# Kernel tuning notes

Measured on AMD Instinct MI355X. Metric: run time of the kernel, lower is better.

## Reference

```python
import math
import jax, jax.numpy as jnp
import numpy as np

B, C, H, W = 4, 256, 64, 64
N_HEAD = 4
GROUPS = 32
EPS = 1e-5


def setup_inputs() -> dict:
    key = jax.random.key(0)
    k1, k2, k3 = jax.random.split(key, 3)
    fan = C  # 1x1 conv fan_in
    bound_qkv = math.sqrt(3.0 * 1.0 / ((fan + 3 * C) / 2))
    x = jax.random.normal(k1, (B, C, H, W), dtype=jnp.float32)
    w_qkv = jax.random.uniform(k2, (3 * C, C), dtype=jnp.float32, minval=-bound_qkv, maxval=bound_qkv)
    # out conv has scale=1e-10 init, but use small random weights for a non-trivial baseline
    w_out = jax.random.normal(k3, (C, C), dtype=jnp.float32) * 0.02
    return {
        "x": x,
        "gn_gamma": jnp.ones((C,), jnp.float32),
        "gn_beta": jnp.zeros((C,), jnp.float32),
        "w_qkv": w_qkv,
        "b_qkv": jnp.zeros((3 * C,), jnp.float32),
        "w_out": w_out,
        "b_out": jnp.zeros((C,), jnp.float32),
    }


def _group_norm(x, gamma, beta):
    b, c, h, w = x.shape
    xr = x.reshape(b, GROUPS, c // GROUPS, h, w)
    mean = xr.mean(axis=(2, 3, 4), keepdims=True)
    var = xr.var(axis=(2, 3, 4), keepdims=True)
    xn = ((xr - mean) * jax.lax.rsqrt(var + EPS)).reshape(b, c, h, w)
    return xn * gamma[None, :, None, None] + beta[None, :, None, None]


def reference(x, gn_gamma, gn_beta, w_qkv, b_qkv, w_out, b_out):
    b, c, h, w = x.shape
    head_dim = c // N_HEAD
    norm = _group_norm(x, gn_gamma, gn_beta)
    # 1x1 conv == channel matmul
    qkv = jnp.einsum('oc,bchw->bohw', w_qkv, norm) + b_qkv[None, :, None, None]
    qkv = qkv.reshape(b, N_HEAD, 3 * head_dim, h, w)
    q, k, v = jnp.split(qkv, 3, axis=2)  # each [b, n, d, h, w]
    # note: original scales by sqrt(channel), NOT sqrt(head_dim)
    attn = jnp.einsum('bnchw,bncyx->bnhwyx', q, k) / math.sqrt(c)
    attn = jax.nn.softmax(attn.reshape(b, N_HEAD, h, w, h * w), axis=-1)
    attn = attn.reshape(b, N_HEAD, h, w, h, w)
    out = jnp.einsum('bnhwyx,bncyx->bnchw', attn, v).reshape(b, c, h, w)
    out = jnp.einsum('oc,bchw->bohw', w_out, out) + b_out[None, :, None, None]
    return (out + x) / np.sqrt(2.0).astype(np.float32)
```

## Files before the change

kernel.cpp:

```cpp
#include <hip/hip_runtime.h>
#include <hip/hip_bf16.h>

#define B_   4
#define C_   256
#define HW_  4096
#define GR_  32
#define CPG_ 8
#define EPS_ 1e-5f
#define QSCALE_ 0.09016844005555897f
#define RSQRT2_ 0.70710678118654752f

typedef short bf16x8 __attribute__((ext_vector_type(8)));
typedef short bf16x4 __attribute__((ext_vector_type(4)));
typedef float f32x4  __attribute__((ext_vector_type(4)));
typedef unsigned short u16x4 __attribute__((ext_vector_type(4)));
typedef unsigned int u32x4 __attribute__((ext_vector_type(4)));

__device__ __forceinline__ unsigned short f2bf(float f) {
  unsigned int x; __builtin_memcpy(&x, &f, 4);
  x = x + 0x7FFFu + ((x >> 16) & 1u);
  return (unsigned short)(x >> 16);
}
__device__ __forceinline__ unsigned int cvtpk(float lo, float hi) {
  unsigned int r;
  asm("v_cvt_pk_bf16_f32 %0, %1, %2" : "=v"(r) : "v"(lo), "v"(hi));
  return r;
}
__device__ __forceinline__ float exp2v(float x) {
  float r;
  asm("v_exp_f32 %0, %1" : "=v"(r) : "v"(x));
  return r;
}

#define GP(p) ((const __attribute__((address_space(1))) void*)(p))
#define LP(p) ((__attribute__((address_space(3))) void*)(p))

__global__ __launch_bounds__(256) void wcvt(const float* __restrict__ wqkv,
                                            const float* __restrict__ bqkv,
                                            const float* __restrict__ wout,
                                            unsigned short* __restrict__ wbf,
                                            float* __restrict__ bias_s) {
  int i = blockIdx.x * 256 + threadIdx.x;
  const int NQ = 768 * 256, NO = 256 * 256;
  if (i < NQ) {
    int o = i >> 8;
    float s = ((o % 192) < 64) ? QSCALE_ : 1.0f;
    wbf[i] = f2bf(wqkv[i] * s);
  } else if (i < NQ + NO) {
    wbf[i] = f2bf(wout[i - NQ]);
  } else if (i < NQ + NO + 768) {
    int o = i - NQ - NO;
    float s = ((o % 192) < 64) ? QSCALE_ : 1.0f;
    bias_s[o] = bqkv[o] * s;
  }
}

__global__ __launch_bounds__(256) void gn_stats(const float* __restrict__ x,
                                                float* __restrict__ stats) {
  int bg = blockIdx.x;
  const float4* p = (const float4*)(x + (size_t)bg * (CPG_ * HW_));
  float s = 0.f, ss = 0.f;
  for (int i = threadIdx.x; i < (CPG_ * HW_ / 4); i += 256) {
    float4 v = p[i];
    s  += v.x + v.y + v.z + v.w;
    ss += v.x * v.x + v.y * v.y + v.z * v.z + v.w * v.w;
  }
  #pragma unroll
  for (int off = 32; off > 0; off >>= 1) {
    s  += __shfl_down(s, off, 64);
    ss += __shfl_down(ss, off, 64);
  }
  __shared__ float rs[4], rss[4];
  int wv = threadIdx.x >> 6;
  if ((threadIdx.x & 63) == 0) { rs[wv] = s; rss[wv] = ss; }
  __syncthreads();
  if (threadIdx.x == 0) {
    float S = rs[0] + rs[1] + rs[2] + rs[3];
    float SS = rss[0] + rss[1] + rss[2] + rss[3];
    float mean = S * (1.f / (CPG_ * HW_));
    float var = SS * (1.f / (CPG_ * HW_)) - mean * mean;
    stats[bg * 2 + 0] = mean;
    stats[bg * 2 + 1] = rsqrtf(var + EPS_);
  }
}

__global__ __launch_bounds__(256) void gn_apply_t(const float* __restrict__ x,
                                                  const float* __restrict__ stats,
                                                  const float* __restrict__ gamma,
                                                  const float* __restrict__ beta,
                                                  unsigned short* __restrict__ xnt) {
  int p0 = blockIdx.x * 64;
  int c0 = blockIdx.y * 64;
  int b  = blockIdx.z;
  int t = threadIdx.x;
  int cl16 = t & 15;
  int row16 = t >> 4;
  __shared__ unsigned short tile[64][66];
  #pragma unroll
  for (int i = 0; i < 4; ++i) {
    int c = c0 + i * 16 + row16;
    int bg = b * GR_ + (c >> 3);
    float mean = stats[bg * 2], rstd = stats[bg * 2 + 1];
    float a = rstd * gamma[c];
    float bb = beta[c] - mean * a;
    float4 v = *(const float4*)&x[((size_t)(b * C_ + c)) * HW_ + p0 + cl16 * 4];
    u16x4 o;
    o[0] = f2bf(v.x * a + bb); o[1] = f2bf(v.y * a + bb);
    o[2] = f2bf(v.z * a + bb); o[3] = f2bf(v.w * a + bb);
    *(u16x4*)&tile[i * 16 + row16][cl16 * 4] = o;
  }
  __syncthreads();
  #pragma unroll
  for (int i = 0; i < 4; ++i) {
    int pp = i * 16 + row16;
    u16x4 o;
    #pragma unroll
    for (int k = 0; k < 4; ++k) o[k] = tile[cl16 * 4 + k][pp];
    *(u16x4*)&xnt[((size_t)b * HW_ + p0 + pp) * C_ + c0 + cl16 * 4] = o;
  }
}

__global__ __launch_bounds__(512) void gemm_qkv(const unsigned short* __restrict__ wbf,
                                                const float* __restrict__ bias_s,
                                                const unsigned short* __restrict__ xnt,
                                                unsigned short* __restrict__ qt,
                                                unsigned short* __restrict__ ktb,
                                                unsigned short* __restrict__ vb) {
  int p0 = blockIdx.x * 64;
  int b  = blockIdx.y;
  int lane = threadIdx.x & 63, wv = threadIdx.x >> 6;
  int cl = lane & 15, g = lane >> 4;

  __shared__ unsigned short bt[64 * 256];

  {
    const unsigned short* xb = xnt + ((size_t)b * HW_ + p0) * C_;
    int rowl = lane >> 5;
    int grl  = lane & 31;
    #pragma unroll
    for (int i = 0; i < 4; ++i) {
      int row = wv * 8 + i * 2 + rowl;
      int sgr = grl ^ (row & 7);
      __builtin_amdgcn_global_load_lds(GP(xb + (size_t)row * C_ + sgr * 8),
                                       LP(bt + (wv * 8 + i * 2) * C_), 16, 0, 0);
    }
  }
  __syncthreads();

  f32x4 z = {0.f, 0.f, 0.f, 0.f};
  f32x4 acc[6][4];
  #pragma unroll
  for (int j = 0; j < 6; ++j)
    #pragma unroll
    for (int nt = 0; nt < 4; ++nt) acc[j][nt] = z;

  const char* btc = (const char*)bt;
  for (int kc = 0; kc < C_; kc += 32) {
    bf16x8 bfr[4];
    #pragma unroll
    for (int nt = 0; nt < 4; ++nt) {
      int row = nt * 16 + cl;
      bfr[nt] = *(const bf16x8*)(btc + row * 512 + ((((kc >> 3) + g) ^ (cl & 7)) << 4));
    }
    #pragma unroll
    for (int j = 0; j < 6; ++j) {
      int rt = wv * 6 + j;
      bf16x8 af = *(const bf16x8*)&wbf[(size_t)(rt * 16 + cl) * C_ + kc + g * 8];
      #pragma unroll
      for (int nt = 0; nt < 4; ++nt)
        acc[j][nt] = __builtin_amdgcn_mfma_f32_16x16x32_bf16(af, bfr[nt], acc[j][nt], 0, 0, 0);
    }
  }

  #pragma unroll
  for (int j = 0; j < 6; ++j) {
    int rt = wv * 6 + j;
    int y = rt >> 2;
    int h = y / 3, type = y - h * 3;
    int bh = b * 4 + h;
    int olocal = (rt & 3) * 16 + g * 4;
    int obase = rt * 16 + g * 4;
    if (type == 2) {
      unsigned short* dst = vb + (size_t)bh * 64 * HW_;
      #pragma unroll
      for (int r = 0; r < 4; ++r) {
        float bv = bias_s[obase + r];
        #pragma unroll
        for (int nt = 0; nt < 4; ++nt)
          dst[(size_t)(olocal + r) * HW_ + p0 + nt * 16 + cl] = f2bf(acc[j][nt][r] + bv);
      }
    } else {
      unsigned short* dst = (type == 0 ? qt : ktb) + (size_t)bh * HW_ * 64;
      #pragma unroll
      for (int nt = 0; nt < 4; ++nt) {
        int p = p0 + nt * 16 + cl;
        u16x4 o4;
        #pragma unroll
        for (int r = 0; r < 4; ++r) o4[r] = f2bf(acc[j][nt][r] + bias_s[obase + r]);
        *(u16x4*)&dst[(size_t)p * 64 + olocal] = o4;
      }
    }
  }
}

__global__ __launch_bounds__(512) void flash_attn(const unsigned short* __restrict__ qt,
                                                  const unsigned short* __restrict__ ktb,
                                                  const unsigned short* __restrict__ vb,
                                                  unsigned short* __restrict__ attnt) {
  int qtile = blockIdx.x;
  int bh = blockIdx.y;
  int lane = threadIdx.x & 63, wv = threadIdx.x >> 6;
  int cl = lane & 15, g = lane >> 4;
  int r8 = lane >> 3;
  int gi = (lane & 7) ^ r8;

  const unsigned short* qtb = qt  + (size_t)bh * HW_ * 64;
  const unsigned short* ktp = ktb + (size_t)bh * HW_ * 64;
  const unsigned short* vbp = vb  + (size_t)bh * 64 * HW_;

  __shared__ unsigned short smem[2][8192];

  int qpix0 = qtile * 256 + wv * 32 + cl;
  bf16x8 qf0[2], qf1[2];
  qf0[0] = *(const bf16x8*)&qtb[(size_t)qpix0 * 64 + g * 8];
  qf0[1] = *(const bf16x8*)&qtb[(size_t)qpix0 * 64 + 32 + g * 8];
  qf1[0] = *(const bf16x8*)&qtb[(size_t)(qpix0 + 16) * 64 + g * 8];
  qf1[1] = *(const bf16x8*)&qtb[(size_t)(qpix0 + 16) * 64 + 32 + g * 8];

  f32x4 z = {0.f, 0.f, 0.f, 0.f};
  f32x4 oacc0[4] = {z, z, z, z};
  f32x4 oacc1[4] = {z, z, z, z};
  f32x4 lfrag0 = z, lfrag1 = z;
  const bf16x4 ones = {(short)0x3F80, (short)0x3F80, (short)0x3F80, (short)0x3F80};

  int rdo = cl * 128 + ((g * 16) ^ ((cl & 7) << 4));
  int vbase = cl * 128 + (g & 1) * 8;
  int vxor  = (cl & 7) << 4;
  int ghalf = g >> 1;

  const unsigned short* kp = ktp + (size_t)(wv * 8 + r8) * 64 + gi * 8;
  const unsigned short* vp = vbp + (size_t)(wv * 8 + r8) * HW_ + gi * 8;

#define STAGE(bi) do {                                                              \
    unsigned short* sb = &smem[bi][0];                                              \
    __builtin_amdgcn_global_load_lds(GP(kp), LP(sb + wv * 512),        16, 0, 0);   \
    __builtin_amdgcn_global_load_lds(GP(vp), LP(sb + 4096 + wv * 512), 16, 0, 0);   \
    kp += 64 * 64;                                                                  \
    vp += 64;                                                                       \
  } while (0)

  STAGE(0);
  __syncthreads();

  int cur = 0;
  for (int t = 0; t < 64; ++t) {
    if (t < 63) STAGE(cur ^ 1);

    const char* kb  = (const char*)&smem[cur][0];
    const char* vbx = (const char*)&smem[cur][4096];

    f32x4 sacc0[4] = {z, z, z, z};
    f32x4 sacc1[4] = {z, z, z, z};
    __builtin_amdgcn_s_setprio(1);
    #pragma unroll
    for (int nt = 0; nt < 4; ++nt) {
      #pragma unroll
      for (int ks = 0; ks < 2; ++ks) {
        bf16x8 kf = *(const bf16x8*)(kb + rdo + nt * 2048 + ks * 64);
        sacc0[nt] = __builtin_amdgcn_mfma_f32_16x16x32_bf16(kf, qf0[ks], sacc0[nt], 0, 0, 0);
        sacc1[nt] = __builtin_amdgcn_mfma_f32_16x16x32_bf16(kf, qf1[ks], sacc1[nt], 0, 0, 0);
      }
    }
    __builtin_amdgcn_s_setprio(0);

    unsigned int pk01a[4], pk23a[4], pk01b[4], pk23b[4];
    #pragma unroll
    for (int nt = 0; nt < 4; ++nt) {
      pk01a[nt] = cvtpk(exp2v(sacc0[nt][0]), exp2v(sacc0[nt][1]));
      pk23a[nt] = cvtpk(exp2v(sacc0[nt][2]), exp2v(sacc0[nt][3]));
      pk01b[nt] = cvtpk(exp2v(sacc1[nt][0]), exp2v(sacc1[nt][1]));
      pk23b[nt] = cvtpk(exp2v(sacc1[nt][2]), exp2v(sacc1[nt][3]));
    }

    __builtin_amdgcn_s_setprio(1);
    #pragma unroll
    for (int nt = 0; nt < 4; ++nt) {
      union { unsigned int u[2]; bf16x4 v; } pb0, pb1;
      pb0.u[0] = pk01a[nt]; pb0.u[1] = pk23a[nt];
      pb1.u[0] = pk01b[nt]; pb1.u[1] = pk23b[nt];
      lfrag0 = __builtin_amdgcn_mfma_f32_16x16x16bf16_1k(ones, pb0.v, lfrag0, 0, 0, 0);
      lfrag1 = __builtin_amdgcn_mfma_f32_16x16x16bf16_1k(ones, pb1.v, lfrag1, 0, 0, 0);
      int gsw = ((nt * 2 + ghalf) << 4) ^ vxor;
      #pragma unroll
      for (int dt = 0; dt < 4; ++dt) {
        bf16x4 vf = *(const bf16x4*)(vbx + dt * 2048 + vbase + gsw);
        oacc0[dt] = __builtin_amdgcn_mfma_f32_16x16x16bf16_1k(vf, pb0.v, oacc0[dt], 0, 0, 0);
        oacc1[dt] = __builtin_amdgcn_mfma_f32_16x16x16bf16_1k(vf, pb1.v, oacc1[dt], 0, 0, 0);
      }
    }
    __builtin_amdgcn_s_setprio(0);
    __syncthreads();
    cur ^= 1;
  }
#undef STAGE

  int b = bh >> 2, h = bh & 3;
  float rl0 = 1.f / lfrag0[0];
  float rl1 = 1.f / lfrag1[0];
  unsigned short* at0 = attnt + ((size_t)b * HW_ + qpix0) * C_ + h * 64;
  unsigned short* at1 = attnt + ((size_t)b * HW_ + qpix0 + 16) * C_ + h * 64;
  #pragma unroll
  for (int dt = 0; dt < 4; ++dt) {
    u16x4 o4a, o4b;
    #pragma unroll
    for (int r = 0; r < 4; ++r) {
      o4a[r] = f2bf(oacc0[dt][r] * rl0);
      o4b[r] = f2bf(oacc1[dt][r] * rl1);
    }
    *(u16x4*)&at0[dt * 16 + g * 4] = o4a;
    *(u16x4*)&at1[dt * 16 + g * 4] = o4b;
  }
}

__global__ __launch_bounds__(512) void gemm_out(const unsigned short* __restrict__ wbf_out,
                                                const float* __restrict__ bias,
                                                const unsigned short* __restrict__ attnt,
                                                const float* __restrict__ x,
                                                float* __restrict__ out) {
  int p0 = blockIdx.x * 64;
  int b  = blockIdx.y;
  int lane = threadIdx.x & 63, wv = threadIdx.x >> 6;
  int cl = lane & 15, g = lane >> 4;

  __shared__ unsigned short bt[64 * 256];

  {
    const unsigned short* ab = attnt + ((size_t)b * HW_ + p0) * C_;
    int rowl = lane >> 5;
    int grl  = lane & 31;
    #pragma unroll
    for (int i = 0; i < 4; ++i) {
      int row = wv * 8 + i * 2 + rowl;
      int sgr = grl ^ (row & 7);
      __builtin_amdgcn_global_load_lds(GP(ab + (size_t)row * C_ + sgr * 8),
                                       LP(bt + (wv * 8 + i * 2) * C_), 16, 0, 0);
    }
  }
  __syncthreads();

  f32x4 z = {0.f, 0.f, 0.f, 0.f};
  f32x4 acc[2][4];
  #pragma unroll
  for (int j = 0; j < 2; ++j)
    #pragma unroll
    for (int nt = 0; nt < 4; ++nt) acc[j][nt] = z;

  const char* btc = (const char*)bt;
  for (int kc = 0; kc < C_; kc += 32) {
    bf16x8 bfr[4];
    #pragma unroll
    for (int nt = 0; nt < 4; ++nt) {
      int row = nt * 16 + cl;
      bfr[nt] = *(const bf16x8*)(btc + row * 512 + ((((kc >> 3) + g) ^ (cl & 7)) << 4));
    }
    #pragma unroll
    for (int j = 0; j < 2; ++j) {
      int rt = wv * 2 + j;
      bf16x8 af = *(const bf16x8*)&wbf_out[(size_t)(rt * 16 + cl) * C_ + kc + g * 8];
      #pragma unroll
      for (int nt = 0; nt < 4; ++nt)
        acc[j][nt] = __builtin_amdgcn_mfma_f32_16x16x32_bf16(af, bfr[nt], acc[j][nt], 0, 0, 0);
    }
  }

  const float* xb = x + (size_t)b * C_ * HW_;
  float* ob = out + (size_t)b * C_ * HW_;
  #pragma unroll
  for (int j = 0; j < 2; ++j) {
    int rt = wv * 2 + j;
    #pragma unroll
    for (int r = 0; r < 4; ++r) {
      int o = rt * 16 + g * 4 + r;
      float bv = bias[o];
      #pragma unroll
      for (int nt = 0; nt < 4; ++nt) {
        int p = p0 + nt * 16 + cl;
        size_t idx = (size_t)o * HW_ + p;
        ob[idx] = (acc[j][nt][r] + bv + xb[idx]) * RSQRT2_;
      }
    }
  }
}

extern "C" void kernel_launch(void* const* d_in, const int* in_sizes, int n_in,
                              void* d_out, int out_size, void* d_ws, size_t ws_size,
                              hipStream_t stream) {
  const float* x     = (const float*)d_in[0];
  const float* gamma = (const float*)d_in[1];
  const float* beta  = (const float*)d_in[2];
  const float* w_qkv = (const float*)d_in[3];
  const float* b_qkv = (const float*)d_in[4];
  const float* w_out = (const float*)d_in[5];
  const float* b_out = (const float*)d_in[6];
  float* out = (float*)d_out;

  char* ws = (char*)d_ws;
  float* stats           = (float*)ws;
  float* bias_s          = (float*)(ws + 1024);
  unsigned short* wbf    = (unsigned short*)(ws + 4096);
  unsigned short* xnt    = (unsigned short*)(ws + 528384);
  unsigned short* qt     = (unsigned short*)(ws + 8916992);
  unsigned short* ktb    = (unsigned short*)(ws + 17305600);
  unsigned short* vb     = (unsigned short*)(ws + 25694208);
  unsigned short* attnt  = xnt;

  wcvt<<<dim3(1028), dim3(256), 0, stream>>>(w_qkv, b_qkv, w_out, wbf, bias_s);
  gn_stats<<<dim3(128), dim3(256), 0, stream>>>(x, stats);
  gn_apply_t<<<dim3(64, 4, 4), dim3(256), 0, stream>>>(x, stats, gamma, beta, xnt);
  gemm_qkv<<<dim3(64, 4), dim3(512), 0, stream>>>(wbf, bias_s, xnt, qt, ktb, vb);
  flash_attn<<<dim3(16, 16), dim3(512), 0, stream>>>(qt, ktb, vb, attnt);
  gemm_out<<<dim3(64, 4), dim3(512), 0, stream>>>(wbf + 768 * 256, b_out, attnt, x, out);
}
```

Measured before the change: 146.6 us.

## Fuse GroupNorm apply into QKV GEMM and compute softmax denominator with VALU adds

```diff
diff --git a/kernel.cpp b/kernel.cpp
--- a/kernel.cpp
+++ b/kernel.cpp
@@ -84,45 +84,12 @@
   }
 }
 
-__global__ __launch_bounds__(256) void gn_apply_t(const float* __restrict__ x,
-                                                  const float* __restrict__ stats,
-                                                  const float* __restrict__ gamma,
-                                                  const float* __restrict__ beta,
-                                                  unsigned short* __restrict__ xnt) {
-  int p0 = blockIdx.x * 64;
-  int c0 = blockIdx.y * 64;
-  int b  = blockIdx.z;
-  int t = threadIdx.x;
-  int cl16 = t & 15;
-  int row16 = t >> 4;
-  __shared__ unsigned short tile[64][66];
-  #pragma unroll
-  for (int i = 0; i < 4; ++i) {
-    int c = c0 + i * 16 + row16;
-    int bg = b * GR_ + (c >> 3);
-    float mean = stats[bg * 2], rstd = stats[bg * 2 + 1];
-    float a = rstd * gamma[c];
-    float bb = beta[c] - mean * a;
-    float4 v = *(const float4*)&x[((size_t)(b * C_ + c)) * HW_ + p0 + cl16 * 4];
-    u16x4 o;
-    o[0] = f2bf(v.x * a + bb); o[1] = f2bf(v.y * a + bb);
-    o[2] = f2bf(v.z * a + bb); o[3] = f2bf(v.w * a + bb);
-    *(u16x4*)&tile[i * 16 + row16][cl16 * 4] = o;
-  }
-  __syncthreads();
-  #pragma unroll
-  for (int i = 0; i < 4; ++i) {
-    int pp = i * 16 + row16;
-    u16x4 o;
-    #pragma unroll
-    for (int k = 0; k < 4; ++k) o[k] = tile[cl16 * 4 + k][pp];
-    *(u16x4*)&xnt[((size_t)b * HW_ + p0 + pp) * C_ + c0 + cl16 * 4] = o;
-  }
-}
-
 __global__ __launch_bounds__(512) void gemm_qkv(const unsigned short* __restrict__ wbf,
                                                 const float* __restrict__ bias_s,
-                                                const unsigned short* __restrict__ xnt,
+                                                const float* __restrict__ x,
+                                                const float* __restrict__ stats,
+                                                const float* __restrict__ gamma,
+                                                const float* __restrict__ beta,
                                                 unsigned short* __restrict__ qt,
                                                 unsigned short* __restrict__ ktb,
                                                 unsigned short* __restrict__ vb) {
@@ -132,20 +99,44 @@
   int cl = lane & 15, g = lane >> 4;
 
   __shared__ unsigned short bt[64 * 256];
+  __shared__ unsigned short scratch[64][68];
 
   {
-    const unsigned short* xb = xnt + ((size_t)b * HW_ + p0) * C_;
-    int rowl = lane >> 5;
-    int grl  = lane & 31;
-    #pragma unroll
-    for (int i = 0; i < 4; ++i) {
-      int row = wv * 8 + i * 2 + rowl;
-      int sgr = grl ^ (row & 7);
-      __builtin_amdgcn_global_load_lds(GP(xb + (size_t)row * C_ + sgr * 8),
-                                       LP(bt + (wv * 8 + i * 2) * C_), 16, 0, 0);
-    }
-  }
-  __syncthreads();
+    int t = threadIdx.x;
+    int cl16 = t & 15;
+    int row32 = t >> 4;
+    const float* xb = x + (size_t)b * C_ * HW_;
+    #pragma unroll
+    for (int cc = 0; cc < 4; ++cc) {
+      int c0 = cc * 64;
+      #pragma unroll
+      for (int i = 0; i < 2; ++i) {
+        int cloc = i * 32 + row32;
+        int c = c0 + cloc;
+        int bg = b * GR_ + (c >> 3);
+        float mean = stats[bg * 2], rstd = stats[bg * 2 + 1];
+        float a = rstd * gamma[c];
+        float bb = beta[c] - mean * a;
+        float4 v = *(const float4*)&xb[(size_t)c * HW_ + p0 + cl16 * 4];
+        u16x4 o;
+        o[0] = f2bf(v.x * a + bb); o[1] = f2bf(v.y * a + bb);
+        o[2] = f2bf(v.z * a + bb); o[3] = f2bf(v.w * a + bb);
+        *(u16x4*)&scratch[cloc][cl16 * 4] = o;
+      }
+      __syncthreads();
+      #pragma unroll
+      for (int i = 0; i < 2; ++i) {
+        int pp = i * 32 + row32;
+        u16x4 o;
+        #pragma unroll
+        for (int k = 0; k < 4; ++k) o[k] = scratch[cl16 * 4 + k][pp];
+        int cbyte = (c0 + cl16 * 4) * 2;
+        int sw = (((cbyte >> 4) ^ (pp & 7)) << 4) | (cbyte & 15);
+        *(u16x4*)((char*)bt + pp * 512 + sw) = o;
+      }
+      __syncthreads();
+    }
+  }
 
   f32x4 z = {0.f, 0.f, 0.f, 0.f};
   f32x4 acc[6][4];
@@ -230,8 +221,7 @@
   f32x4 z = {0.f, 0.f, 0.f, 0.f};
   f32x4 oacc0[4] = {z, z, z, z};
   f32x4 oacc1[4] = {z, z, z, z};
-  f32x4 lfrag0 = z, lfrag1 = z;
-  const bf16x4 ones = {(short)0x3F80, (short)0x3F80, (short)0x3F80, (short)0x3F80};
+  f32x4 lacc0 = z, lacc1 = z;
 
   int rdo = cl * 128 + ((g * 16) ^ ((cl & 7) << 4));
   int vbase = cl * 128 + (g & 1) * 8;
@@ -276,10 +266,17 @@
     unsigned int pk01a[4], pk23a[4], pk01b[4], pk23b[4];
     #pragma unroll
     for (int nt = 0; nt < 4; ++nt) {
-      pk01a[nt] = cvtpk(exp2v(sacc0[nt][0]), exp2v(sacc0[nt][1]));
-      pk23a[nt] = cvtpk(exp2v(sacc0[nt][2]), exp2v(sacc0[nt][3]));
-      pk01b[nt] = cvtpk(exp2v(sacc1[nt][0]), exp2v(sacc1[nt][1]));
-      pk23b[nt] = cvtpk(exp2v(sacc1[nt][2]), exp2v(sacc1[nt][3]));
+      f32x4 pa, pbv;
+      pa[0] = exp2v(sacc0[nt][0]); pa[1] = exp2v(sacc0[nt][1]);
+      pa[2] = exp2v(sacc0[nt][2]); pa[3] = exp2v(sacc0[nt][3]);
+      pbv[0] = exp2v(sacc1[nt][0]); pbv[1] = exp2v(sacc1[nt][1]);
+      pbv[2] = exp2v(sacc1[nt][2]); pbv[3] = exp2v(sacc1[nt][3]);
+      lacc0 += pa;
+      lacc1 += pbv;
+      pk01a[nt] = cvtpk(pa[0], pa[1]);
+      pk23a[nt] = cvtpk(pa[2], pa[3]);
+      pk01b[nt] = cvtpk(pbv[0], pbv[1]);
+      pk23b[nt] = cvtpk(pbv[2], pbv[3]);
     }
 
     __builtin_amdgcn_s_setprio(1);
@@ -288,8 +285,6 @@
       union { unsigned int u[2]; bf16x4 v; } pb0, pb1;
       pb0.u[0] = pk01a[nt]; pb0.u[1] = pk23a[nt];
       pb1.u[0] = pk01b[nt]; pb1.u[1] = pk23b[nt];
-      lfrag0 = __builtin_amdgcn_mfma_f32_16x16x16bf16_1k(ones, pb0.v, lfrag0, 0, 0, 0);
-      lfrag1 = __builtin_amdgcn_mfma_f32_16x16x16bf16_1k(ones, pb1.v, lfrag1, 0, 0, 0);
       int gsw = ((nt * 2 + ghalf) << 4) ^ vxor;
       #pragma unroll
       for (int dt = 0; dt < 4; ++dt) {
@@ -304,9 +299,16 @@
   }
 #undef STAGE
 
+  float l0 = lacc0[0] + lacc0[1] + lacc0[2] + lacc0[3];
+  l0 += __shfl_xor(l0, 16, 64);
+  l0 += __shfl_xor(l0, 32, 64);
+  float l1 = lacc1[0] + lacc1[1] + lacc1[2] + lacc1[3];
+  l1 += __shfl_xor(l1, 16, 64);
+  l1 += __shfl_xor(l1, 32, 64);
+
   int b = bh >> 2, h = bh & 3;
-  float rl0 = 1.f / lfrag0[0];
-  float rl1 = 1.f / lfrag1[0];
+  float rl0 = 1.f / l0;
+  float rl1 = 1.f / l1;
   unsigned short* at0 = attnt + ((size_t)b * HW_ + qpix0) * C_ + h * 64;
   unsigned short* at1 = attnt + ((size_t)b * HW_ + qpix0 + 16) * C_ + h * 64;
   #pragma unroll
@@ -408,16 +410,14 @@
   float* stats           = (float*)ws;
   float* bias_s          = (float*)(ws + 1024);
   unsigned short* wbf    = (unsigned short*)(ws + 4096);
-  unsigned short* xnt    = (unsigned short*)(ws + 528384);
+  unsigned short* attnt  = (unsigned short*)(ws + 528384);
   unsigned short* qt     = (unsigned short*)(ws + 8916992);
   unsigned short* ktb    = (unsigned short*)(ws + 17305600);
   unsigned short* vb     = (unsigned short*)(ws + 25694208);
-  unsigned short* attnt  = xnt;
 
   wcvt<<<dim3(1028), dim3(256), 0, stream>>>(w_qkv, b_qkv, w_out, wbf, bias_s);
   gn_stats<<<dim3(128), dim3(256), 0, stream>>>(x, stats);
-  gn_apply_t<<<dim3(64, 4, 4), dim3(256), 0, stream>>>(x, stats, gamma, beta, xnt);
-  gemm_qkv<<<dim3(64, 4), dim3(512), 0, stream>>>(wbf, bias_s, xnt, qt, ktb, vb);
+  gemm_qkv<<<dim3(64, 4), dim3(512), 0, stream>>>(wbf, bias_s, x, stats, gamma, beta, qt, ktb, vb);
   flash_attn<<<dim3(16, 16), dim3(512), 0, stream>>>(qt, ktb, vb, attnt);
   gemm_out<<<dim3(64, 4), dim3(512), 0, stream>>>(wbf + 768 * 256, b_out, attnt, x, out);
 }
```

Result: faster. 143.4 us (-2.1%).
